# Kernel optimization log

Measured on AMD Instinct MI355X. Metric: run time of the kernel, lower is better.

The kernel has to match this reference:

```python
import jax, jax.numpy as jnp
import numpy as np
from jax import lax


def setup_inputs() -> dict:
    key = jax.random.key(0)
    k1, k2 = jax.random.split(key)
    B, C, H, W = 8, 16, 128, 128
    rate = 2
    hs = H // rate
    hw = hs * hs
    x = jax.random.normal(k1, (B, C, H, W), dtype=jnp.float32)
    scores = jax.random.normal(k2, (B, hw, hw), dtype=jnp.float32)
    alpha = jnp.ones((1,), dtype=jnp.float32)
    return {"x": x, "scores": scores, "alpha": alpha}


def reference(x, scores, alpha):
    B, C, H, W = x.shape
    P = scores.shape[2]              # hw = hs*ws
    hs = int(np.sqrt(P))
    ws = hs
    rate = H // hs
    vk = 2 * rate                    # vksize
    pad = rate // 2                  # vpadding (ReplicationPad2d)

    # --- extract_patches: replication pad + unfold(kernel=vk, stride=rate) ---
    xp = jnp.pad(x, ((0, 0), (0, 0), (pad, pad), (pad, pad)), mode='edge')
    ii = (jnp.arange(hs) * rate)[:, None] + jnp.arange(vk)[None, :]   # [hs, vk]
    jj = (jnp.arange(ws) * rate)[:, None] + jnp.arange(vk)[None, :]   # [ws, vk]
    # gather overlapping patches: [B, C, hs, vk, ws, vk]
    V = xp[:, :, ii][:, :, :, :, jj]
    # -> [B, hs*ws, C, vk, vk] matching torch layout (B, hs, ws, C, vk, vk)
    V = V.transpose(0, 2, 4, 1, 3, 5).reshape(B, hs * ws, C, vk, vk)

    # --- scores: permute(0,2,1) then reshape to per-patch spatial maps ---
    S = scores.transpose(0, 2, 1).reshape(B, P, hs, ws)  # channel p = key index

    # --- grouped conv_transpose2d(stride=rate, padding=pad, groups=B) ---
    # torch conv_transpose2d == lhs-dilated conv with flipped, transposed kernel
    # and padding (vk - 1 - pad) per side; vmapped over batch (one group each).
    w_pad = vk - 1 - pad

    def conv_t(s, v):
        # s: [P, hs, ws] (input channels = patches); v: [P, C, vk, vk]
        w = jnp.flip(v, axis=(-2, -1)).transpose(1, 0, 2, 3)  # [C, P, vk, vk]
        out = lax.conv_general_dilated(
            s[None], w,
            window_strides=(1, 1),
            padding=[(w_pad, w_pad), (w_pad, w_pad)],
            lhs_dilation=(rate, rate),
            dimension_numbers=('NCHW', 'OIHW', 'NCHW'))
        return out[0]  # [C, H, W]

    y = jax.vmap(conv_t)(S, V) / 4.0  # [B, C, H, W]
    return x + y * alpha
```

## Files before the change

kernel.cpp:

```cpp
#include <hip/hip_runtime.h>
#include <hip/hip_bf16.h>

typedef float f32x4 __attribute__((ext_vector_type(4)));
typedef short bf16x8 __attribute__((ext_vector_type(8)));
typedef unsigned short us8 __attribute__((ext_vector_type(8)));

__device__ __forceinline__ unsigned short f2bf(float f) {
  union { float f; unsigned u; } v; v.f = f;
  return (unsigned short)((v.u + 0x8000u) >> 16);
}
__device__ __forceinline__ float bf2f(unsigned short u) {
  union { unsigned u; float f; } v; v.u = ((unsigned)u) << 16;
  return v.f;
}

__global__ __launch_bounds__(256) void prep_vmat(const float* __restrict__ x,
                                                 unsigned short* __restrict__ vmatT) {
  int t = blockIdx.x * 256 + threadIdx.x;
  int pc = t & 511;
  int n  = (t >> 9) & 255;
  int b  = t >> 17;
  int c = n >> 4, u = (n >> 2) & 3, v = n & 3;
  int pi = pc >> 3;
  int pj0 = (pc & 7) << 3;
  int row = 2 * pi + u - 1;
  row = row < 0 ? 0 : (row > 127 ? 127 : row);
  const float* xr = x + ((size_t)(b * 16 + c) * 128 + row) * 128;
  us8 o;
#pragma unroll
  for (int e = 0; e < 8; ++e) {
    int col = 2 * (pj0 + e) + v - 1;
    col = col < 0 ? 0 : (col > 127 ? 127 : col);
    o[e] = f2bf(xr[col]);
  }
  *reinterpret_cast<us8*>(vmatT + (size_t)t * 8) = o;
}

__global__ __launch_bounds__(256) void gemm_scores_vmat(
    const float* __restrict__ scores,
    const unsigned short* __restrict__ vmatT,
    unsigned short* __restrict__ Amat) {
  __shared__ unsigned short ldsB[2][16384];

  int bid = blockIdx.x;
  int nb = ((bid & 7) << 6) | (bid >> 3);
  int batch = nb >> 6;
  int qb = (nb & 63) << 6;
  const int phase = (bid >> 3) & 63;

  const int t = threadIdx.x;
  const int lane = t & 63;
  const int wq = t >> 6;
  const int l15 = lane & 15, l16 = lane >> 4;

  const float* aLane =
      scores + ((size_t)(batch * 4096 + qb + wq * 16 + l15)) * 4096 + l16 * 8;
  const unsigned short* Vb = vmatT + (size_t)batch * 256 * 4096;

  const unsigned short* bSrc[8];
  int bDst[8];
#pragma unroll
  for (int i = 0; i < 8; ++i) {
    int c = t + i * 256;
    int gs = (c & 7) ^ ((c >> 3) & 7);
    bSrc[i] = Vb + (size_t)(c >> 3) * 4096 + gs * 8;
    bDst[i] = c * 8;
  }
  const int pos0 = (l16 ^ (l15 & 7)) << 3;

  f32x4 acc[16];
#pragma unroll
  for (int ni = 0; ni < 16; ++ni) acc[ni] = (f32x4){0.f, 0.f, 0.f, 0.f};

  f32x4 rE[4], rO[4];
  bf16x8 fe0, fe1, fo0, fo1;

#define SB __builtin_amdgcn_sched_barrier(0)
#define STAGE_B(kt, bufi)                                                     \
  {                                                                           \
    int kp_ = ((kt) + phase) & 63;                                            \
    _Pragma("unroll") for (int i = 0; i < 8; ++i)                             \
        __builtin_amdgcn_global_load_lds(                                     \
            (const __attribute__((address_space(1))) void*)(bSrc[i] + (size_t)kp_ * 64), \
            (__attribute__((address_space(3))) void*)&ldsB[bufi][bDst[i]],    \
            16, 0, 0);                                                        \
  }
#define LOAD_A(kt, rr)                                                        \
  {                                                                           \
    int kp_ = ((kt) + phase) & 63;                                            \
    const float* ap_ = aLane + (size_t)kp_ * 64;                              \
    rr[0] = *(const f32x4*)(ap_);                                             \
    rr[1] = *(const f32x4*)(ap_ + 4);                                         \
    rr[2] = *(const f32x4*)(ap_ + 32);                                        \
    rr[3] = *(const f32x4*)(ap_ + 36);                                        \
  }
#define CONV(rr, fa0, fa1)                                                    \
  {                                                                           \
    _Pragma("unroll") for (int e = 0; e < 4; ++e) {                           \
      fa0[e] = (short)f2bf(rr[0][e]); fa0[e + 4] = (short)f2bf(rr[1][e]);     \
      fa1[e] = (short)f2bf(rr[2][e]); fa1[e + 4] = (short)f2bf(rr[3][e]);     \
    }                                                                         \
  }
#define MFMAS(fa0, fa1, bufi)                                                 \
  {                                                                           \
    _Pragma("unroll") for (int ni = 0; ni < 16; ++ni) {                       \
      bf16x8 bv = *(const bf16x8*)(&ldsB[bufi][0] +                           \
                                   (ni * 16 + l15) * 64 + pos0);              \
      acc[ni] = __builtin_amdgcn_mfma_f32_16x16x32_bf16(fa0, bv, acc[ni],     \
                                                        0, 0, 0);             \
    }                                                                         \
    _Pragma("unroll") for (int ni = 0; ni < 16; ++ni) {                       \
      bf16x8 bv = *(const bf16x8*)(&ldsB[bufi][0] +                           \
                                   (ni * 16 + l15) * 64 + (pos0 ^ 32));      \
      acc[ni] = __builtin_amdgcn_mfma_f32_16x16x32_bf16(fa1, bv, acc[ni],     \
                                                        0, 0, 0);             \
    }                                                                         \
  }

  LOAD_A(0, rE);
  SB;
  STAGE_B(0, 0);
  SB;
  LOAD_A(1, rO);
  SB;
  asm volatile("s_waitcnt vmcnt(4)" ::: "memory");
  SB;
  __builtin_amdgcn_s_barrier();
  SB;

  for (int kt = 0; kt < 64; kt += 2) {
    CONV(rE, fe0, fe1);
    SB;
    STAGE_B(kt + 1, 1);
    SB;
    LOAD_A(kt + 2, rE);
    SB;
    MFMAS(fe0, fe1, 0);
    asm volatile("s_waitcnt vmcnt(4)" ::: "memory");
    SB;
    __builtin_amdgcn_s_barrier();
    SB;
    CONV(rO, fo0, fo1);
    SB;
    STAGE_B(kt + 2, 0);
    SB;
    LOAD_A(kt + 3, rO);
    SB;
    MFMAS(fo0, fo1, 1);
    asm volatile("s_waitcnt vmcnt(4)" ::: "memory");
    SB;
    __builtin_amdgcn_s_barrier();
    SB;
  }

  asm volatile("" ::"v"(rE[0][0]), "v"(rE[1][0]), "v"(rE[2][0]), "v"(rE[3][0]),
               "v"(rO[0][0]), "v"(rO[1][0]), "v"(rO[2][0]), "v"(rO[3][0]));

#undef SB
#undef STAGE_B
#undef LOAD_A
#undef CONV
#undef MFMAS

  unsigned short* Ao = Amat + ((size_t)(batch * 4096 + qb + wq * 16)) * 256;
#pragma unroll
  for (int ni = 0; ni < 16; ++ni)
#pragma unroll
    for (int j = 0; j < 4; ++j)
      Ao[(size_t)(l16 * 4 + j) * 256 + ni * 16 + l15] = f2bf(acc[ni][j]);
}

__global__ __launch_bounds__(256) void epilogue_kernel(
    const float* __restrict__ x, const unsigned short* __restrict__ Amat,
    const float* __restrict__ alpha, float* __restrict__ out) {
  int b = blockIdx.x >> 7;
  int h = blockIdx.x & 127;
  int t = threadIdx.x;
  int w = t & 127;
  int cg = t >> 7;

  int ihi = (h + 1) >> 1, u_hi = (h + 1) & 1;
  int jhi = (w + 1) >> 1, v_hi = (w + 1) & 1;
  bool vi_hi = (ihi <= 63), vi_lo = (ihi >= 1);
  bool vj_hi = (jhi <= 63), vj_lo = (jhi >= 1);

  float al = alpha[0] * 0.25f;
  const unsigned short* Ab = Amat + (size_t)b * 4096 * 256;

#pragma unroll
  for (int cc = 0; cc < 8; ++cc) {
    int c = cg * 8 + cc;
    float s = 0.f;
    if (vi_hi) {
      const unsigned short* Ar = Ab + (size_t)(ihi * 64) * 256 + c * 16 + u_hi * 4;
      if (vj_hi) s += bf2f(Ar[jhi * 256 + v_hi]);
      if (vj_lo) s += bf2f(Ar[(jhi - 1) * 256 + v_hi + 2]);
    }
    if (vi_lo) {
      const unsigned short* Ar = Ab + (size_t)((ihi - 1) * 64) * 256 + c * 16 + (u_hi + 2) * 4;
      if (vj_hi) s += bf2f(Ar[jhi * 256 + v_hi]);
      if (vj_lo) s += bf2f(Ar[(jhi - 1) * 256 + v_hi + 2]);
    }
    size_t xi = (((size_t)b * 16 + c) * 128 + h) * 128 + w;
    out[xi] = x[xi] + al * s;
  }
}

extern "C" void kernel_launch(void* const* d_in, const int* in_sizes, int n_in,
                              void* d_out, int out_size, void* d_ws, size_t ws_size,
                              hipStream_t stream) {
  const float* x      = (const float*)d_in[0];
  const float* scores = (const float*)d_in[1];
  const float* alpha  = (const float*)d_in[2];
  float* out = (float*)d_out;

  unsigned short* vmatT = (unsigned short*)d_ws;
  unsigned short* Amat  = (unsigned short*)((char*)d_ws + (size_t)16 * 1024 * 1024);

  prep_vmat<<<4096, 256, 0, stream>>>(x, vmatT);
  gemm_scores_vmat<<<512, 256, 0, stream>>>(scores, vmatT, Amat);
  epilogue_kernel<<<1024, 256, 0, stream>>>(x, Amat, alpha, out);
}
```

Baseline: 190.3 us.

## Retile GEMM warps into 2x2 grid to halve LDS B-fragment reads

Changes each wave's output tile in the scores×Vmat GEMM from 16 rows × 256 cols to 32 rows × 128 cols (2×2 wave grid). Each B fragment read from LDS now feeds two MFMAs, halving LDS read traffic per MFMA. A-register loads per wave double, with waitcnt adjusted. Also adds a min-blocks-per-CU hint of 2 to launch bounds, which may constrain register allocation.

New measurement: 243.4 us. 1.28x slower.

```diff
diff --git a/kernel.cpp b/kernel.cpp
--- a/kernel.cpp
+++ b/kernel.cpp
@@ -36,7 +36,7 @@
   *reinterpret_cast<us8*>(vmatT + (size_t)t * 8) = o;
 }
 
-__global__ __launch_bounds__(256) void gemm_scores_vmat(
+__global__ __launch_bounds__(256, 2) void gemm_scores_vmat(
     const float* __restrict__ scores,
     const unsigned short* __restrict__ vmatT,
     unsigned short* __restrict__ Amat) {
@@ -51,10 +51,11 @@
   const int t = threadIdx.x;
   const int lane = t & 63;
   const int wq = t >> 6;
+  const int wm = wq >> 1, wn = wq & 1;
   const int l15 = lane & 15, l16 = lane >> 4;
 
   const float* aLane =
-      scores + ((size_t)(batch * 4096 + qb + wq * 16 + l15)) * 4096 + l16 * 8;
+      scores + ((size_t)(batch * 4096 + qb + wm * 32 + l15)) * 4096 + l16 * 8;
   const unsigned short* Vb = vmatT + (size_t)batch * 256 * 4096;
 
   const unsigned short* bSrc[8];
@@ -67,13 +68,16 @@
     bDst[i] = c * 8;
   }
   const int pos0 = (l16 ^ (l15 & 7)) << 3;
-
-  f32x4 acc[16];
-#pragma unroll
-  for (int ni = 0; ni < 16; ++ni) acc[ni] = (f32x4){0.f, 0.f, 0.f, 0.f};
-
-  f32x4 rE[4], rO[4];
-  bf16x8 fe0, fe1, fo0, fo1;
+  const int bRow = wn * 128 + l15;
+
+  f32x4 acc[2][8];
+#pragma unroll
+  for (int m = 0; m < 2; ++m)
+#pragma unroll
+    for (int ni = 0; ni < 8; ++ni) acc[m][ni] = (f32x4){0.f, 0.f, 0.f, 0.f};
+
+  f32x4 rE[8], rO[8];
+  bf16x8 fe[2][2], fo[2][2];
 
 #define SB __builtin_amdgcn_sched_barrier(0)
 #define STAGE_B(kt, bufi)                                                     \
@@ -93,28 +97,32 @@
     rr[1] = *(const f32x4*)(ap_ + 4);                                         \
     rr[2] = *(const f32x4*)(ap_ + 32);                                        \
     rr[3] = *(const f32x4*)(ap_ + 36);                                        \
-  }
-#define CONV(rr, fa0, fa1)                                                    \
-  {                                                                           \
-    _Pragma("unroll") for (int e = 0; e < 4; ++e) {                           \
-      fa0[e] = (short)f2bf(rr[0][e]); fa0[e + 4] = (short)f2bf(rr[1][e]);     \
-      fa1[e] = (short)f2bf(rr[2][e]); fa1[e + 4] = (short)f2bf(rr[3][e]);     \
+    const float* aq_ = ap_ + (size_t)16 * 4096;                               \
+    rr[4] = *(const f32x4*)(aq_);                                             \
+    rr[5] = *(const f32x4*)(aq_ + 4);                                         \
+    rr[6] = *(const f32x4*)(aq_ + 32);                                        \
+    rr[7] = *(const f32x4*)(aq_ + 36);                                        \
+  }
+#define CONV(rr, ff)                                                          \
+  {                                                                           \
+    _Pragma("unroll") for (int m = 0; m < 2; ++m)                             \
+        _Pragma("unroll") for (int ks = 0; ks < 2; ++ks)                      \
+            _Pragma("unroll") for (int e = 0; e < 4; ++e) {                   \
+      ff[m][ks][e]     = (short)f2bf(rr[m * 4 + ks * 2][e]);                  \
+      ff[m][ks][e + 4] = (short)f2bf(rr[m * 4 + ks * 2 + 1][e]);              \
     }                                                                         \
   }
-#define MFMAS(fa0, fa1, bufi)                                                 \
-  {                                                                           \
-    _Pragma("unroll") for (int ni = 0; ni < 16; ++ni) {                       \
+#define MFMAS(ff, bufi)                                                       \
+  {                                                                           \
+    _Pragma("unroll") for (int ks = 0; ks < 2; ++ks)                          \
+        _Pragma("unroll") for (int ni = 0; ni < 8; ++ni) {                    \
       bf16x8 bv = *(const bf16x8*)(&ldsB[bufi][0] +                           \
-                                   (ni * 16 + l15) * 64 + pos0);              \
-      acc[ni] = __builtin_amdgcn_mfma_f32_16x16x32_bf16(fa0, bv, acc[ni],     \
-                                                        0, 0, 0);             \
+                                   (bRow + ni * 16) * 64 + (pos0 ^ (ks * 32))); \
+      acc[0][ni] = __builtin_amdgcn_mfma_f32_16x16x32_bf16(ff[0][ks], bv,     \
+                                                           acc[0][ni], 0, 0, 0); \
+      acc[1][ni] = __builtin_amdgcn_mfma_f32_16x16x32_bf16(ff[1][ks], bv,     \
+                                                           acc[1][ni], 0, 0, 0); \
     }                                                                         \
-    _Pragma("unroll") for (int ni = 0; ni < 16; ++ni) {                       \
-      bf16x8 bv = *(const bf16x8*)(&ldsB[bufi][0] +                           \
-                                   (ni * 16 + l15) * 64 + (pos0 ^ 32));      \
-      acc[ni] = __builtin_amdgcn_mfma_f32_16x16x32_bf16(fa1, bv, acc[ni],     \
-                                                        0, 0, 0);             \
-    }                                                                         \
   }
 
   LOAD_A(0, rE);
@@ -123,38 +131,40 @@
   SB;
   LOAD_A(1, rO);
   SB;
-  asm volatile("s_waitcnt vmcnt(4)" ::: "memory");
+  asm volatile("s_waitcnt vmcnt(8)" ::: "memory");
   SB;
   __builtin_amdgcn_s_barrier();
   SB;
 
   for (int kt = 0; kt < 64; kt += 2) {
-    CONV(rE, fe0, fe1);
+    CONV(rE, fe);
     SB;
     STAGE_B(kt + 1, 1);
     SB;
     LOAD_A(kt + 2, rE);
     SB;
-    MFMAS(fe0, fe1, 0);
-    asm volatile("s_waitcnt vmcnt(4)" ::: "memory");
+    MFMAS(fe, 0);
+    asm volatile("s_waitcnt vmcnt(8)" ::: "memory");
     SB;
     __builtin_amdgcn_s_barrier();
     SB;
-    CONV(rO, fo0, fo1);
+    CONV(rO, fo);
     SB;
     STAGE_B(kt + 2, 0);
     SB;
     LOAD_A(kt + 3, rO);
     SB;
-    MFMAS(fo0, fo1, 1);
-    asm volatile("s_waitcnt vmcnt(4)" ::: "memory");
+    MFMAS(fo, 1);
+    asm volatile("s_waitcnt vmcnt(8)" ::: "memory");
     SB;
     __builtin_amdgcn_s_barrier();
     SB;
   }
 
   asm volatile("" ::"v"(rE[0][0]), "v"(rE[1][0]), "v"(rE[2][0]), "v"(rE[3][0]),
-               "v"(rO[0][0]), "v"(rO[1][0]), "v"(rO[2][0]), "v"(rO[3][0]));
+               "v"(rE[4][0]), "v"(rE[5][0]), "v"(rE[6][0]), "v"(rE[7][0]),
+               "v"(rO[0][0]), "v"(rO[1][0]), "v"(rO[2][0]), "v"(rO[3][0]),
+               "v"(rO[4][0]), "v"(rO[5][0]), "v"(rO[6][0]), "v"(rO[7][0]));
 
 #undef SB
 #undef STAGE_B
@@ -162,12 +172,16 @@
 #undef CONV
 #undef MFMAS
 
-  unsigned short* Ao = Amat + ((size_t)(batch * 4096 + qb + wq * 16)) * 256;
-#pragma unroll
-  for (int ni = 0; ni < 16; ++ni)
-#pragma unroll
-    for (int j = 0; j < 4; ++j)
-      Ao[(size_t)(l16 * 4 + j) * 256 + ni * 16 + l15] = f2bf(acc[ni][j]);
+  unsigned short* Ao =
+      Amat + ((size_t)(batch * 4096 + qb + wm * 32)) * 256 + wn * 128;
+#pragma unroll
+  for (int m = 0; m < 2; ++m)
+#pragma unroll
+    for (int ni = 0; ni < 8; ++ni)
+#pragma unroll
+      for (int j = 0; j < 4; ++j)
+        Ao[(size_t)(m * 16 + l16 * 4 + j) * 256 + ni * 16 + l15] =
+            f2bf(acc[m][ni][j]);
 }
 
 __global__ __launch_bounds__(256) void epilogue_kernel(
```

## Split GEMM K dimension in two and sum partials in epilogue

Applied to the files above, without the earlier changes.

Splits the 4096-long K reduction of the scores×V GEMM into two halves, doubling the grid to 1024 blocks, each with a 32-wide K tile and half the LDS buffer. Each half writes its own bf16 partial matrix, and the epilogue reads both and adds them. The goal is more concurrent blocks and higher occupancy (launch bounds now request 4 blocks per SM) on a GEMM that had only 512 blocks. The cost is twice the intermediate write and read traffic, extra rounding from storing two bf16 partials, and a bigger workspace.

New measurement: 298.7 us. +57.0%, slower.

```diff
diff --git a/kernel.cpp b/kernel.cpp
--- a/kernel.cpp
+++ b/kernel.cpp
@@ -36,85 +36,76 @@
   *reinterpret_cast<us8*>(vmatT + (size_t)t * 8) = o;
 }
 
-__global__ __launch_bounds__(256) void gemm_scores_vmat(
+__global__ __launch_bounds__(256, 4) void gemm_scores_vmat(
     const float* __restrict__ scores,
     const unsigned short* __restrict__ vmatT,
-    unsigned short* __restrict__ Amat) {
-  __shared__ unsigned short ldsB[2][16384];
+    unsigned short* __restrict__ AmatP) {
+  __shared__ unsigned short ldsB[2][8192];
 
   int bid = blockIdx.x;
-  int nb = ((bid & 7) << 6) | (bid >> 3);
-  int batch = nb >> 6;
-  int qb = (nb & 63) << 6;
-  const int phase = (bid >> 3) & 63;
+  int batch = bid & 7;
+  int inner = bid >> 3;
+  int qb = (inner & 63) << 6;
+  int ksp = inner >> 6;
+  const int phase = inner & 63;
 
   const int t = threadIdx.x;
   const int lane = t & 63;
   const int wq = t >> 6;
   const int l15 = lane & 15, l16 = lane >> 4;
 
-  const float* aLane =
-      scores + ((size_t)(batch * 4096 + qb + wq * 16 + l15)) * 4096 + l16 * 8;
-  const unsigned short* Vb = vmatT + (size_t)batch * 256 * 4096;
-
-  const unsigned short* bSrc[8];
-  int bDst[8];
-#pragma unroll
-  for (int i = 0; i < 8; ++i) {
+  const size_t kbase = (size_t)ksp * 2048;
+  const float* aLane = scores +
+      ((size_t)(batch * 4096 + qb + wq * 16 + l15)) * 4096 + kbase + l16 * 8;
+  const unsigned short* Vb = vmatT + (size_t)batch * 256 * 4096 + kbase;
+
+  const unsigned short* bSrc[4];
+#pragma unroll
+  for (int i = 0; i < 4; ++i) {
     int c = t + i * 256;
-    int gs = (c & 7) ^ ((c >> 3) & 7);
-    bSrc[i] = Vb + (size_t)(c >> 3) * 4096 + gs * 8;
-    bDst[i] = c * 8;
-  }
-  const int pos0 = (l16 ^ (l15 & 7)) << 3;
+    int gs = (c & 3) ^ ((c >> 3) & 3);
+    bSrc[i] = Vb + (size_t)(c >> 2) * 4096 + gs * 8;
+  }
+  const int rsw = (l16 ^ ((l15 >> 1) & 3)) << 3;
 
   f32x4 acc[16];
 #pragma unroll
   for (int ni = 0; ni < 16; ++ni) acc[ni] = (f32x4){0.f, 0.f, 0.f, 0.f};
 
-  f32x4 rE[4], rO[4];
-  bf16x8 fe0, fe1, fo0, fo1;
+  f32x4 rE[2], rO[2];
+  bf16x8 fe, fo;
 
 #define SB __builtin_amdgcn_sched_barrier(0)
 #define STAGE_B(kt, bufi)                                                     \
   {                                                                           \
     int kp_ = ((kt) + phase) & 63;                                            \
-    _Pragma("unroll") for (int i = 0; i < 8; ++i)                             \
+    _Pragma("unroll") for (int i = 0; i < 4; ++i)                             \
         __builtin_amdgcn_global_load_lds(                                     \
-            (const __attribute__((address_space(1))) void*)(bSrc[i] + (size_t)kp_ * 64), \
-            (__attribute__((address_space(3))) void*)&ldsB[bufi][bDst[i]],    \
+            (const __attribute__((address_space(1))) void*)(bSrc[i] + (size_t)kp_ * 32), \
+            (__attribute__((address_space(3))) void*)&ldsB[bufi][(t + i * 256) * 8], \
             16, 0, 0);                                                        \
   }
 #define LOAD_A(kt, rr)                                                        \
   {                                                                           \
     int kp_ = ((kt) + phase) & 63;                                            \
-    const float* ap_ = aLane + (size_t)kp_ * 64;                              \
+    const float* ap_ = aLane + (size_t)kp_ * 32;                              \
     rr[0] = *(const f32x4*)(ap_);                                             \
     rr[1] = *(const f32x4*)(ap_ + 4);                                         \
-    rr[2] = *(const f32x4*)(ap_ + 32);                                        \
-    rr[3] = *(const f32x4*)(ap_ + 36);                                        \
-  }
-#define CONV(rr, fa0, fa1)                                                    \
+  }
+#define CONV(rr, fa)                                                          \
   {                                                                           \
     _Pragma("unroll") for (int e = 0; e < 4; ++e) {                           \
-      fa0[e] = (short)f2bf(rr[0][e]); fa0[e + 4] = (short)f2bf(rr[1][e]);     \
-      fa1[e] = (short)f2bf(rr[2][e]); fa1[e + 4] = (short)f2bf(rr[3][e]);     \
+      fa[e] = (short)f2bf(rr[0][e]); fa[e + 4] = (short)f2bf(rr[1][e]);       \
     }                                                                         \
   }
-#define MFMAS(fa0, fa1, bufi)                                                 \
+#define MFMAS(fa, bufi)                                                       \
   {                                                                           \
     _Pragma("unroll") for (int ni = 0; ni < 16; ++ni) {                       \
       bf16x8 bv = *(const bf16x8*)(&ldsB[bufi][0] +                           \
-                                   (ni * 16 + l15) * 64 + pos0);              \
-      acc[ni] = __builtin_amdgcn_mfma_f32_16x16x32_bf16(fa0, bv, acc[ni],     \
+                                   (ni * 16 + l15) * 32 + rsw);               \
+      acc[ni] = __builtin_amdgcn_mfma_f32_16x16x32_bf16(fa, bv, acc[ni],      \
                                                         0, 0, 0);             \
     }                                                                         \
-    _Pragma("unroll") for (int ni = 0; ni < 16; ++ni) {                       \
-      bf16x8 bv = *(const bf16x8*)(&ldsB[bufi][0] +                           \
-                                   (ni * 16 + l15) * 64 + (pos0 ^ 32));      \
-      acc[ni] = __builtin_amdgcn_mfma_f32_16x16x32_bf16(fa1, bv, acc[ni],     \
-                                                        0, 0, 0);             \
-    }                                                                         \
   }
 
   LOAD_A(0, rE);
@@ -123,38 +114,37 @@
   SB;
   LOAD_A(1, rO);
   SB;
-  asm volatile("s_waitcnt vmcnt(4)" ::: "memory");
+  asm volatile("s_waitcnt vmcnt(2)" ::: "memory");
   SB;
   __builtin_amdgcn_s_barrier();
   SB;
 
   for (int kt = 0; kt < 64; kt += 2) {
-    CONV(rE, fe0, fe1);
+    CONV(rE, fe);
     SB;
     STAGE_B(kt + 1, 1);
     SB;
     LOAD_A(kt + 2, rE);
     SB;
-    MFMAS(fe0, fe1, 0);
-    asm volatile("s_waitcnt vmcnt(4)" ::: "memory");
+    MFMAS(fe, 0);
+    asm volatile("s_waitcnt vmcnt(2)" ::: "memory");
     SB;
     __builtin_amdgcn_s_barrier();
     SB;
-    CONV(rO, fo0, fo1);
+    CONV(rO, fo);
     SB;
     STAGE_B(kt + 2, 0);
     SB;
     LOAD_A(kt + 3, rO);
     SB;
-    MFMAS(fo0, fo1, 1);
-    asm volatile("s_waitcnt vmcnt(4)" ::: "memory");
+    MFMAS(fo, 1);
+    asm volatile("s_waitcnt vmcnt(2)" ::: "memory");
     SB;
     __builtin_amdgcn_s_barrier();
     SB;
   }
 
-  asm volatile("" ::"v"(rE[0][0]), "v"(rE[1][0]), "v"(rE[2][0]), "v"(rE[3][0]),
-               "v"(rO[0][0]), "v"(rO[1][0]), "v"(rO[2][0]), "v"(rO[3][0]));
+  asm volatile("" ::"v"(rE[0][0]), "v"(rE[1][0]), "v"(rO[0][0]), "v"(rO[1][0]));
 
 #undef SB
 #undef STAGE_B
@@ -162,7 +152,8 @@
 #undef CONV
 #undef MFMAS
 
-  unsigned short* Ao = Amat + ((size_t)(batch * 4096 + qb + wq * 16)) * 256;
+  unsigned short* Ao = AmatP + (size_t)ksp * 8 * 4096 * 256 +
+                       ((size_t)(batch * 4096 + qb + wq * 16)) * 256;
 #pragma unroll
   for (int ni = 0; ni < 16; ++ni)
 #pragma unroll
@@ -171,7 +162,7 @@
 }
 
 __global__ __launch_bounds__(256) void epilogue_kernel(
-    const float* __restrict__ x, const unsigned short* __restrict__ Amat,
+    const float* __restrict__ x, const unsigned short* __restrict__ AmatP,
     const float* __restrict__ alpha, float* __restrict__ out) {
   int b = blockIdx.x >> 7;
   int h = blockIdx.x & 127;
@@ -185,21 +176,34 @@
   bool vj_hi = (jhi <= 63), vj_lo = (jhi >= 1);
 
   float al = alpha[0] * 0.25f;
-  const unsigned short* Ab = Amat + (size_t)b * 4096 * 256;
+  const unsigned short* A0 = AmatP + (size_t)b * 4096 * 256;
+  const unsigned short* A1 = A0 + (size_t)8 * 4096 * 256;
 
 #pragma unroll
   for (int cc = 0; cc < 8; ++cc) {
     int c = cg * 8 + cc;
     float s = 0.f;
     if (vi_hi) {
-      const unsigned short* Ar = Ab + (size_t)(ihi * 64) * 256 + c * 16 + u_hi * 4;
-      if (vj_hi) s += bf2f(Ar[jhi * 256 + v_hi]);
-      if (vj_lo) s += bf2f(Ar[(jhi - 1) * 256 + v_hi + 2]);
+      size_t base = (size_t)(ihi * 64) * 256 + c * 16 + u_hi * 4;
+      if (vj_hi) {
+        size_t i0 = base + jhi * 256 + v_hi;
+        s += bf2f(A0[i0]) + bf2f(A1[i0]);
+      }
+      if (vj_lo) {
+        size_t i0 = base + (jhi - 1) * 256 + v_hi + 2;
+        s += bf2f(A0[i0]) + bf2f(A1[i0]);
+      }
     }
     if (vi_lo) {
-      const unsigned short* Ar = Ab + (size_t)((ihi - 1) * 64) * 256 + c * 16 + (u_hi + 2) * 4;
-      if (vj_hi) s += bf2f(Ar[jhi * 256 + v_hi]);
-      if (vj_lo) s += bf2f(Ar[(jhi - 1) * 256 + v_hi + 2]);
+      size_t base = (size_t)((ihi - 1) * 64) * 256 + c * 16 + (u_hi + 2) * 4;
+      if (vj_hi) {
+        size_t i0 = base + jhi * 256 + v_hi;
+        s += bf2f(A0[i0]) + bf2f(A1[i0]);
+      }
+      if (vj_lo) {
+        size_t i0 = base + (jhi - 1) * 256 + v_hi + 2;
+        s += bf2f(A0[i0]) + bf2f(A1[i0]);
+      }
     }
     size_t xi = (((size_t)b * 16 + c) * 128 + h) * 128 + w;
     out[xi] = x[xi] + al * s;
@@ -215,9 +219,9 @@
   float* out = (float*)d_out;
 
   unsigned short* vmatT = (unsigned short*)d_ws;
-  unsigned short* Amat  = (unsigned short*)((char*)d_ws + (size_t)16 * 1024 * 1024);
+  unsigned short* AmatP = (unsigned short*)((char*)d_ws + (size_t)16 * 1024 * 1024);
 
   prep_vmat<<<4096, 256, 0, stream>>>(x, vmatT);
-  gemm_scores_vmat<<<512, 256, 0, stream>>>(scores, vmatT, Amat);
-  epilogue_kernel<<<1024, 256, 0, stream>>>(x, Amat, alpha, out);
-}
+  gemm_scores_vmat<<<1024, 256, 0, stream>>>(scores, vmatT, AmatP);
+  epilogue_kernel<<<1024, 256, 0, stream>>>(x, AmatP, alpha, out);
+}
```

## Double GEMM block size and deepen load pipeline to four stages

Applied to the files above, without the earlier changes.

Reorganizes the scores×V GEMM into 512-thread blocks covering 128 query rows per batch, so each LDS-staged V tile is shared by twice as many rows. The software pipeline grows from two to four LDS buffers and four A-register prefetch stages, keeping more global loads in flight. The cost is more LDS and register pressure per block, with fewer, larger blocks (one per CU) and possible spills under the tightened launch bounds.

Result: faster. 172.9 us (-9.1%).

```diff
diff --git a/kernel.cpp b/kernel.cpp
--- a/kernel.cpp
+++ b/kernel.cpp
@@ -36,17 +36,16 @@
   *reinterpret_cast<us8*>(vmatT + (size_t)t * 8) = o;
 }
 
-__global__ __launch_bounds__(256) void gemm_scores_vmat(
+__global__ __launch_bounds__(512, 2) void gemm_scores_vmat(
     const float* __restrict__ scores,
     const unsigned short* __restrict__ vmatT,
     unsigned short* __restrict__ Amat) {
-  __shared__ unsigned short ldsB[2][16384];
+  __shared__ unsigned short ldsB[4][16384];
 
   int bid = blockIdx.x;
-  int nb = ((bid & 7) << 6) | (bid >> 3);
-  int batch = nb >> 6;
-  int qb = (nb & 63) << 6;
-  const int phase = (bid >> 3) & 63;
+  int batch = bid & 7;
+  int qb = (bid >> 3) << 7;
+  const int phase = ((bid >> 3) * 2) & 63;
 
   const int t = threadIdx.x;
   const int lane = t & 63;
@@ -57,14 +56,12 @@
       scores + ((size_t)(batch * 4096 + qb + wq * 16 + l15)) * 4096 + l16 * 8;
   const unsigned short* Vb = vmatT + (size_t)batch * 256 * 4096;
 
-  const unsigned short* bSrc[8];
-  int bDst[8];
-#pragma unroll
-  for (int i = 0; i < 8; ++i) {
-    int c = t + i * 256;
+  const unsigned short* bSrc[4];
+#pragma unroll
+  for (int i = 0; i < 4; ++i) {
+    int c = t + i * 512;
     int gs = (c & 7) ^ ((c >> 3) & 7);
     bSrc[i] = Vb + (size_t)(c >> 3) * 4096 + gs * 8;
-    bDst[i] = c * 8;
   }
   const int pos0 = (l16 ^ (l15 & 7)) << 3;
 
@@ -72,17 +69,17 @@
 #pragma unroll
   for (int ni = 0; ni < 16; ++ni) acc[ni] = (f32x4){0.f, 0.f, 0.f, 0.f};
 
-  f32x4 rE[4], rO[4];
-  bf16x8 fe0, fe1, fo0, fo1;
+  f32x4 r0[4], r1[4], r2[4], r3[4];
+  bf16x8 fa0, fa1;
 
 #define SB __builtin_amdgcn_sched_barrier(0)
 #define STAGE_B(kt, bufi)                                                     \
   {                                                                           \
     int kp_ = ((kt) + phase) & 63;                                            \
-    _Pragma("unroll") for (int i = 0; i < 8; ++i)                             \
+    _Pragma("unroll") for (int i = 0; i < 4; ++i)                             \
         __builtin_amdgcn_global_load_lds(                                     \
             (const __attribute__((address_space(1))) void*)(bSrc[i] + (size_t)kp_ * 64), \
-            (__attribute__((address_space(3))) void*)&ldsB[bufi][bDst[i]],    \
+            (__attribute__((address_space(3))) void*)&ldsB[bufi][(t + i * 512) * 8], \
             16, 0, 0);                                                        \
   }
 #define LOAD_A(kt, rr)                                                        \
@@ -94,14 +91,14 @@
     rr[2] = *(const f32x4*)(ap_ + 32);                                        \
     rr[3] = *(const f32x4*)(ap_ + 36);                                        \
   }
-#define CONV(rr, fa0, fa1)                                                    \
+#define CONV(rr)                                                              \
   {                                                                           \
     _Pragma("unroll") for (int e = 0; e < 4; ++e) {                           \
       fa0[e] = (short)f2bf(rr[0][e]); fa0[e + 4] = (short)f2bf(rr[1][e]);     \
       fa1[e] = (short)f2bf(rr[2][e]); fa1[e + 4] = (short)f2bf(rr[3][e]);     \
     }                                                                         \
   }
-#define MFMAS(fa0, fa1, bufi)                                                 \
+#define MFMAS(bufi)                                                           \
   {                                                                           \
     _Pragma("unroll") for (int ni = 0; ni < 16; ++ni) {                       \
       bf16x8 bv = *(const bf16x8*)(&ldsB[bufi][0] +                           \
@@ -116,51 +113,55 @@
                                                         0, 0, 0);             \
     }                                                                         \
   }
-
-  LOAD_A(0, rE);
-  SB;
+#define BODY(m, kt, rr)                                                       \
+  {                                                                           \
+    CONV(rr);                                      \
+    SB;                                                                       \
+    STAGE_B((kt) + 2, ((m) + 2) & 3);                                         \
+    SB;                                                                       \
+    LOAD_A((kt) + 4, rr);                                                     \
+    SB;                                                                       \
+    MFMAS(m);                                                                 \
+    SB;                                                                       \
+    asm volatile("s_waitcnt vmcnt(12)" ::: "memory");                         \
+    SB;                                                                       \
+    __builtin_amdgcn_s_barrier();                                             \
+    SB;                                                                       \
+  }
+
   STAGE_B(0, 0);
   SB;
-  LOAD_A(1, rO);
-  SB;
-  asm volatile("s_waitcnt vmcnt(4)" ::: "memory");
+  LOAD_A(0, r0);
+  SB;
+  LOAD_A(1, r1);
+  SB;
+  LOAD_A(2, r2);
+  SB;
+  STAGE_B(1, 1);
+  SB;
+  LOAD_A(3, r3);
+  SB;
+  asm volatile("s_waitcnt vmcnt(12)" ::: "memory");
   SB;
   __builtin_amdgcn_s_barrier();
   SB;
 
-  for (int kt = 0; kt < 64; kt += 2) {
-    CONV(rE, fe0, fe1);
-    SB;
-    STAGE_B(kt + 1, 1);
-    SB;
-    LOAD_A(kt + 2, rE);
-    SB;
-    MFMAS(fe0, fe1, 0);
-    asm volatile("s_waitcnt vmcnt(4)" ::: "memory");
-    SB;
-    __builtin_amdgcn_s_barrier();
-    SB;
-    CONV(rO, fo0, fo1);
-    SB;
-    STAGE_B(kt + 2, 0);
-    SB;
-    LOAD_A(kt + 3, rO);
-    SB;
-    MFMAS(fo0, fo1, 1);
-    asm volatile("s_waitcnt vmcnt(4)" ::: "memory");
-    SB;
-    __builtin_amdgcn_s_barrier();
-    SB;
-  }
-
-  asm volatile("" ::"v"(rE[0][0]), "v"(rE[1][0]), "v"(rE[2][0]), "v"(rE[3][0]),
-               "v"(rO[0][0]), "v"(rO[1][0]), "v"(rO[2][0]), "v"(rO[3][0]));
+  for (int kt = 0; kt < 64; kt += 4) {
+    BODY(0, kt, r0);
+    BODY(1, kt + 1, r1);
+    BODY(2, kt + 2, r2);
+    BODY(3, kt + 3, r3);
+  }
+
+  asm volatile("" ::"v"(r0[0][0]), "v"(r1[0][0]), "v"(r2[0][0]), "v"(r3[0][0]),
+               "v"(r0[3][0]), "v"(r1[3][0]), "v"(r2[3][0]), "v"(r3[3][0]));
 
 #undef SB
 #undef STAGE_B
 #undef LOAD_A
 #undef CONV
 #undef MFMAS
+#undef BODY
 
   unsigned short* Ao = Amat + ((size_t)(batch * 4096 + qb + wq * 16)) * 256;
 #pragma unroll
@@ -218,6 +219,6 @@
   unsigned short* Amat  = (unsigned short*)((char*)d_ws + (size_t)16 * 1024 * 1024);
 
   prep_vmat<<<4096, 256, 0, stream>>>(x, vmatT);
-  gemm_scores_vmat<<<512, 256, 0, stream>>>(scores, vmatT, Amat);
+  gemm_scores_vmat<<<256, 512, 0, stream>>>(scores, vmatT, Amat);
   epilogue_kernel<<<1024, 256, 0, stream>>>(x, Amat, alpha, out);
 }
```
